# Optimization experiments

Hardware: AMD Instinct MI355X
Metric: run time of the kernel (lower is better)

## Reference

```python
import jax, jax.numpy as jnp
import numpy as np

N_NODES = 50000
N_EDGES = 800000
N_SUPPORTS = 2
D_IN = 512
D_OUT = 128


def setup_inputs() -> dict:
    key = jax.random.key(0)
    ks = jax.random.split(key, 6)
    x = jax.random.normal(ks[0], (N_NODES, D_IN), dtype=jnp.float32)
    kernels = jax.random.normal(ks[1], (N_SUPPORTS, D_IN, D_OUT), dtype=jnp.float32) * 0.05
    bias = jax.random.normal(ks[2], (D_OUT,), dtype=jnp.float32) * 0.05
    adj_vals = jax.random.uniform(ks[3], (N_SUPPORTS, N_EDGES), dtype=jnp.float32)
    adj_rows = jax.random.randint(ks[4], (N_SUPPORTS, N_EDGES), 0, N_NODES, dtype=jnp.int32)
    adj_cols = jax.random.randint(ks[5], (N_SUPPORTS, N_EDGES), 0, N_NODES, dtype=jnp.int32)
    return {"x": x, "kernels": kernels, "bias": bias,
            "adj_vals": adj_vals, "adj_rows": adj_rows, "adj_cols": adj_cols}


def _spmm(vals, rows, cols, dense):
    # COO sparse [N,N] @ dense [N,F] -> [N,F]
    gathered = vals[:, None] * dense[cols]            # [E, F]
    return jax.ops.segment_sum(gathered, rows, num_segments=N_NODES)


def reference(x, kernels, bias, adj_vals, adj_rows, adj_cols):
    # dropout rate = 0.0 -> identity
    out = jnp.zeros((N_NODES, D_OUT), dtype=x.dtype)
    for s in range(N_SUPPORTS):  # small fixed number of supports
        pre_sup = x @ kernels[s]                      # [N, D_OUT]
        out = out + _spmm(adj_vals[s], adj_rows[s], adj_cols[s], pre_sup)
    out = out + bias
    return jax.nn.relu(out)
```

## Files before the change

### kernel.cpp

```cpp
#include <hip/hip_runtime.h>

#define N_NODES 50000
#define N_EDGES 800000
#define D_IN    512
#define D_OUT   128
#define N_SUP   2
#define N_COLS  (N_SUP * D_OUT)
#define BINS    (N_SUP * N_NODES)
#define NB_S    196
#define NB      (N_SUP * NB_S)
#define CAP     4608
#define CHUNK   4096
#define NCHUNK  ((N_EDGES + CHUNK - 1) / CHUNK)

typedef __attribute__((ext_vector_type(8))) __bf16 bf16x8;
typedef __attribute__((ext_vector_type(4))) float  f32x4;

__global__ __launch_bounds__(256) void convert_w(const float* __restrict__ w,
                                                 __bf16* __restrict__ wt2) {
    const int g = blockIdx.x * 256 + threadIdx.x;
    if (g >= (D_IN / 8) * N_COLS) return;
    const int kq = g >> 8;
    const int n  = g & 255;
    const int s  = n >> 7;
    const int np = n & 127;
    bf16x8 v;
#pragma unroll
    for (int j = 0; j < 8; ++j) {
        const int k = kq * 8 + j;
        v[j] = (__bf16)w[((size_t)s * D_IN + k) * D_OUT + np];
    }
    *(bf16x8*)(wt2 + (size_t)g * 8) = v;
}

__global__ __launch_bounds__(256) void gemm_bf16(const float* __restrict__ x,
                                                 const __bf16* __restrict__ wt2,
                                                 __bf16* __restrict__ pre) {
    __shared__ __align__(16) __bf16 Bs[2048 * 8];

    const int t    = threadIdx.x;
    const int lane = t & 63;
    const int w    = t >> 6;
    const int l15  = lane & 15;
    const int quad = lane >> 4;

    const int rbase = blockIdx.x * 64 + w * 16;
    int arow = rbase + l15;
    if (arow >= N_NODES) arow = N_NODES - 1;
    const float* aptr = x + (size_t)arow * D_IN + quad * 8;

    f32x4 acc[16];
#pragma unroll
    for (int i = 0; i < 16; ++i) acc[i] = (f32x4)0.f;

    for (int kb = 0; kb < 8; ++kb) {
        const __bf16* gsrc = wt2 + ((size_t)kb * 2048 + w * 64 + lane) * 8;
#pragma unroll
        for (int i = 0; i < 8; ++i) {
            __builtin_amdgcn_global_load_lds(
                (const __attribute__((address_space(1))) unsigned int*)(gsrc + (size_t)i * 2048),
                (__attribute__((address_space(3))) unsigned int*)(&Bs[(i * 256 + w * 64) * 8]),
                16, 0, 0);
        }
        bf16x8 afrag[2];
#pragma unroll
        for (int kk = 0; kk < 2; ++kk) {
            const float* ap = aptr + kb * 64 + kk * 32;
            float4 f0 = *(const float4*)(ap);
            float4 f1 = *(const float4*)(ap + 4);
            bf16x8 a;
            a[0] = (__bf16)f0.x; a[1] = (__bf16)f0.y;
            a[2] = (__bf16)f0.z; a[3] = (__bf16)f0.w;
            a[4] = (__bf16)f1.x; a[5] = (__bf16)f1.y;
            a[6] = (__bf16)f1.z; a[7] = (__bf16)f1.w;
            afrag[kk] = a;
        }
        __syncthreads();

#pragma unroll
        for (int kk = 0; kk < 2; ++kk) {
            const __bf16* bbase = &Bs[((kk * 4 + quad) * 256 + l15) * 8];
#pragma unroll
            for (int ct = 0; ct < 16; ++ct) {
                bf16x8 b = *(const bf16x8*)(bbase + ct * 128);
                acc[ct] = __builtin_amdgcn_mfma_f32_16x16x32_bf16(afrag[kk], b, acc[ct], 0, 0, 0);
            }
        }
        __syncthreads();
    }

#pragma unroll
    for (int ct = 0; ct < 16; ++ct) {
        const int col = ct * 16 + l15;
        const int s   = col >> 7;
        const int cp  = col & 127;
#pragma unroll
        for (int r = 0; r < 4; ++r) {
            const int row = rbase + quad * 4 + r;
            if (row < N_NODES)
                pre[((size_t)s * N_NODES + row) * D_OUT + cp] = (__bf16)acc[ct][r];
        }
    }
}

__global__ __launch_bounds__(256) void scatter_coarse(const float* __restrict__ adj_vals,
                                                      const int* __restrict__ adj_rows,
                                                      const int* __restrict__ adj_cols,
                                                      int* __restrict__ gcursor,
                                                      uint2* __restrict__ coarse) {
    __shared__ int lh[NB_S];
    __shared__ int lbase[NB_S];
    const int s = blockIdx.y;
    const int t = threadIdx.x;
    if (t < NB_S) lh[t] = 0;
    __syncthreads();

    const int e0 = blockIdx.x * CHUNK;
    int   rr[16]; int cc[16]; float vv[16];
#pragma unroll
    for (int i = 0; i < 16; ++i) {
        const int e = e0 + i * 256 + t;
        if (e < N_EDGES) {
            const size_t src = (size_t)s * N_EDGES + e;
            rr[i] = adj_rows[src];
            cc[i] = adj_cols[src];
            vv[i] = adj_vals[src];
            atomicAdd(&lh[rr[i] >> 8], 1);
        } else {
            rr[i] = -1; cc[i] = 0; vv[i] = 0.f;
        }
    }
    __syncthreads();
    if (t < NB_S) {
        lbase[t] = lh[t] ? atomicAdd(&gcursor[s * NB_S + t], lh[t]) : 0;
        lh[t] = 0;
    }
    __syncthreads();
#pragma unroll
    for (int i = 0; i < 16; ++i) {
        if (rr[i] >= 0) {
            const int b    = rr[i] >> 8;
            const int pos  = lbase[b] + atomicAdd(&lh[b], 1);
            if (pos < CAP)
                coarse[(size_t)(s * NB_S + b) * CAP + pos] =
                    make_uint2(__float_as_uint(vv[i]),
                               ((unsigned)(rr[i] & 255) << 16) | (unsigned)cc[i]);
        }
    }
}

__global__ __launch_bounds__(256) void scatter_fine(const uint2* __restrict__ coarse,
                                                    const int* __restrict__ gcursor,
                                                    uint2* __restrict__ sorted,
                                                    int* __restrict__ row_off,
                                                    int* __restrict__ row_cnt) {
    __shared__ int rh[256];
    __shared__ int sd[256];
    __shared__ int rbs[256];
    __shared__ int rc[256];
    const int bk = blockIdx.x;
    const int s  = blockIdx.y;
    const int t  = threadIdx.x;
    const int bkt = s * NB_S + bk;
    const int b0  = bkt * CAP;
    const int cnt = min(gcursor[bkt], CAP);

    rh[t] = 0; rc[t] = 0;
    __syncthreads();
    for (int i = t; i < cnt; i += 256) {
        const uint2 ed = coarse[b0 + i];
        atomicAdd(&rh[ed.y >> 16], 1);
    }
    __syncthreads();
    const int myc = rh[t];
    sd[t] = myc;
    __syncthreads();
    for (int off = 1; off < 256; off <<= 1) {
        const int a = (t >= off) ? sd[t - off] : 0;
        __syncthreads();
        sd[t] += a;
        __syncthreads();
    }
    const int ex  = sd[t] - myc;
    const int row = (bk << 8) + t;
    if (row < N_NODES) {
        row_off[s * N_NODES + row] = b0 + ex;
        row_cnt[s * N_NODES + row] = myc;
    }
    rbs[t] = b0 + ex;
    __syncthreads();
    for (int i = t; i < cnt; i += 256) {
        const uint2 ed = coarse[b0 + i];
        const int   rl = ed.y >> 16;
        const int rank = atomicAdd(&rc[rl], 1);
        sorted[rbs[rl] + rank] = make_uint2(ed.x, ed.y & 0xFFFFu);
    }
}

__global__ __launch_bounds__(256) void gather_spmm(const int* __restrict__ row_off,
                                                   const int* __restrict__ row_cnt,
                                                   const uint2* __restrict__ sorted,
                                                   const uint4* __restrict__ pre_q,
                                                   const float* __restrict__ bias,
                                                   float* __restrict__ out) {
    const int lane = threadIdx.x & 63;
    const int q    = lane >> 4;
    const int fl   = lane & 15;
    const int row  = blockIdx.x * 4 + (threadIdx.x >> 6);
    if (row >= N_NODES) return;

    float a[8];
#pragma unroll
    for (int k = 0; k < 8; ++k) a[k] = 0.f;

#pragma unroll
    for (int s = 0; s < N_SUP; ++s) {
        const int bin   = s * N_NODES + row;
        const int start = row_off[bin];
        const int cnt   = row_cnt[bin];
        const uint4* psup = pre_q + (size_t)s * N_NODES * 16 + fl;

        for (int e0 = 0; e0 < cnt; e0 += 64) {
            const int m = min(64, cnt - e0);
            int   c = 0;
            float v = 0.f;
            if (lane < m) {
                const uint2 ed = sorted[start + e0 + lane];
                v = __uint_as_float(ed.x);
                c = (int)ed.y;
            }
            const int steps = (m + 3) >> 2;

            auto step = [&](int jj) {
                const int   idx = (jj < m) ? jj : 0;
                float vj = __shfl(v, idx);
                const int cj = __shfl(c, idx);
                if (jj >= m) vj = 0.f;
                const uint4 p = psup[(size_t)cj * 16];
                a[0] += vj * __uint_as_float(p.x << 16);
                a[1] += vj * __uint_as_float(p.x & 0xffff0000u);
                a[2] += vj * __uint_as_float(p.y << 16);
                a[3] += vj * __uint_as_float(p.y & 0xffff0000u);
                a[4] += vj * __uint_as_float(p.z << 16);
                a[5] += vj * __uint_as_float(p.z & 0xffff0000u);
                a[6] += vj * __uint_as_float(p.w << 16);
                a[7] += vj * __uint_as_float(p.w & 0xffff0000u);
            };
            int jj = 0;
            for (; jj + 1 < steps; jj += 2) {
                step(jj * 4 + q);
                step(jj * 4 + 4 + q);
            }
            if (jj < steps) step(jj * 4 + q);
        }
    }

#pragma unroll
    for (int k = 0; k < 8; ++k) {
        a[k] += __shfl_xor(a[k], 16);
        a[k] += __shfl_xor(a[k], 32);
    }

    if (lane < 16) {
        const float4 b0 = *(const float4*)(bias + fl * 8);
        const float4 b1 = *(const float4*)(bias + fl * 8 + 4);
        float4 o0, o1;
        o0.x = fmaxf(a[0] + b0.x, 0.f);
        o0.y = fmaxf(a[1] + b0.y, 0.f);
        o0.z = fmaxf(a[2] + b0.z, 0.f);
        o0.w = fmaxf(a[3] + b0.w, 0.f);
        o1.x = fmaxf(a[4] + b1.x, 0.f);
        o1.y = fmaxf(a[5] + b1.y, 0.f);
        o1.z = fmaxf(a[6] + b1.z, 0.f);
        o1.w = fmaxf(a[7] + b1.w, 0.f);
        float* dst = out + (size_t)row * D_OUT + fl * 8;
        *(float4*)(dst)     = o0;
        *(float4*)(dst + 4) = o1;
    }
}

extern "C" void kernel_launch(void* const* d_in, const int* in_sizes, int n_in,
                              void* d_out, int out_size, void* d_ws, size_t ws_size,
                              hipStream_t stream) {
    const float* x        = (const float*)d_in[0];
    const float* kernels  = (const float*)d_in[1];
    const float* bias     = (const float*)d_in[2];
    const float* adj_vals = (const float*)d_in[3];
    const int*   adj_rows = (const int*)d_in[4];
    const int*   adj_cols = (const int*)d_in[5];
    float* out = (float*)d_out;

    char* ws = (char*)d_ws;
    size_t off = 0;
    auto alloc = [&](size_t bytes) {
        char* p = ws + off;
        off += (bytes + 255) & ~(size_t)255;
        return p;
    };
    __bf16* pre    = (__bf16*)alloc(sizeof(__bf16) * N_SUP * N_NODES * D_OUT);
    __bf16* wt2    = (__bf16*)alloc(sizeof(__bf16) * D_IN * N_COLS);
    uint2*  coarse = (uint2*) alloc(sizeof(uint2)  * NB * CAP);
    uint2*  sorted = (uint2*) alloc(sizeof(uint2)  * NB * CAP);
    int*    row_off = (int*)alloc(sizeof(int) * BINS);
    int*    row_cnt = (int*)alloc(sizeof(int) * BINS);
    int*    gcursor = (int*)alloc(sizeof(int) * NB);

    convert_w<<<(D_IN / 8) * N_COLS / 256, 256, 0, stream>>>(kernels, wt2);
    gemm_bf16<<<(N_NODES + 63) / 64, 256, 0, stream>>>(x, wt2, pre);

    hipMemsetAsync(gcursor, 0, sizeof(int) * NB, stream);
    dim3 gc(NCHUNK, N_SUP);
    scatter_coarse<<<gc, 256, 0, stream>>>(adj_vals, adj_rows, adj_cols, gcursor, coarse);
    dim3 gf(NB_S, N_SUP);
    scatter_fine<<<gf, 256, 0, stream>>>(coarse, gcursor, sorted, row_off, row_cnt);

    gather_spmm<<<(N_NODES + 3) / 4, 256, 0, stream>>>(row_off, row_cnt, sorted,
                                                       (const uint4*)pre, bias, out);
}
```

Baseline: 283.8 us.

## Stage bucket scatters in LDS for coalesced writes; fold cursor reset into convert_w

Both scatter passes now sort their edges by bucket or row inside shared memory first, then write them out contiguously. This replaces random per-edge global stores with coalesced ones. scatter_fine now loads its edges into registers once instead of reading coarse twice, and the gcursor memset is folded into convert_w to save one launch. The cost is much larger LDS use per block (32 KB and 36 KB), which lowers occupancy, and extra block-wide scans and barriers.

```diff
diff --git a/kernel.cpp b/kernel.cpp
--- a/kernel.cpp
+++ b/kernel.cpp
@@ -17,8 +17,10 @@
 typedef __attribute__((ext_vector_type(4))) float  f32x4;
 
 __global__ __launch_bounds__(256) void convert_w(const float* __restrict__ w,
-                                                 __bf16* __restrict__ wt2) {
+                                                 __bf16* __restrict__ wt2,
+                                                 int* __restrict__ gcursor) {
     const int g = blockIdx.x * 256 + threadIdx.x;
+    if (g < NB) gcursor[g] = 0;
     if (g >= (D_IN / 8) * N_COLS) return;
     const int kq = g >> 8;
     const int n  = g & 255;
@@ -108,11 +110,16 @@
                                                       const int* __restrict__ adj_cols,
                                                       int* __restrict__ gcursor,
                                                       uint2* __restrict__ coarse) {
-    __shared__ int lh[NB_S];
+    __shared__ int hist[NB_S];
+    __shared__ int excl[NB_S];
     __shared__ int lbase[NB_S];
+    __shared__ int rankc[NB_S];
+    __shared__ int sc[256];
+    __shared__ uint2 buf[CHUNK];
+
     const int s = blockIdx.y;
     const int t = threadIdx.x;
-    if (t < NB_S) lh[t] = 0;
+    if (t < NB_S) { hist[t] = 0; rankc[t] = 0; }
     __syncthreads();
 
     const int e0 = blockIdx.x * CHUNK;
@@ -125,27 +132,45 @@
             rr[i] = adj_rows[src];
             cc[i] = adj_cols[src];
             vv[i] = adj_vals[src];
-            atomicAdd(&lh[rr[i] >> 8], 1);
+            atomicAdd(&hist[rr[i] >> 8], 1);
         } else {
             rr[i] = -1; cc[i] = 0; vv[i] = 0.f;
         }
     }
     __syncthreads();
+
+    sc[t] = (t < NB_S) ? hist[t] : 0;
+    __syncthreads();
+    for (int off = 1; off < 256; off <<= 1) {
+        const int a = (t >= off) ? sc[t - off] : 0;
+        __syncthreads();
+        sc[t] += a;
+        __syncthreads();
+    }
     if (t < NB_S) {
-        lbase[t] = lh[t] ? atomicAdd(&gcursor[s * NB_S + t], lh[t]) : 0;
-        lh[t] = 0;
-    }
-    __syncthreads();
+        excl[t]  = sc[t] - hist[t];
+        lbase[t] = hist[t] ? atomicAdd(&gcursor[s * NB_S + t], hist[t]) : 0;
+    }
+    __syncthreads();
+
 #pragma unroll
     for (int i = 0; i < 16; ++i) {
         if (rr[i] >= 0) {
-            const int b    = rr[i] >> 8;
-            const int pos  = lbase[b] + atomicAdd(&lh[b], 1);
-            if (pos < CAP)
-                coarse[(size_t)(s * NB_S + b) * CAP + pos] =
-                    make_uint2(__float_as_uint(vv[i]),
-                               ((unsigned)(rr[i] & 255) << 16) | (unsigned)cc[i]);
-        }
+            const int b   = rr[i] >> 8;
+            const int pos = excl[b] + atomicAdd(&rankc[b], 1);
+            buf[pos] = make_uint2(__float_as_uint(vv[i]),
+                                  ((unsigned)rr[i] << 16) | (unsigned)cc[i]);
+        }
+    }
+    __syncthreads();
+
+    const int total = min(e0 + CHUNK, N_EDGES) - e0;
+    for (int i = t; i < total; i += 256) {
+        const uint2 ed = buf[i];
+        const int b   = ed.y >> 24;
+        const int dst = lbase[b] + (i - excl[b]);
+        if (dst < CAP)
+            coarse[(size_t)(s * NB_S + b) * CAP + dst] = ed;
     }
 }
 
@@ -156,22 +181,31 @@
                                                     int* __restrict__ row_cnt) {
     __shared__ int rh[256];
     __shared__ int sd[256];
-    __shared__ int rbs[256];
+    __shared__ int rex[256];
     __shared__ int rc[256];
+    __shared__ uint2 buf[CAP];
+
     const int bk = blockIdx.x;
     const int s  = blockIdx.y;
     const int t  = threadIdx.x;
     const int bkt = s * NB_S + bk;
-    const int b0  = bkt * CAP;
+    const size_t b0 = (size_t)bkt * CAP;
     const int cnt = min(gcursor[bkt], CAP);
 
     rh[t] = 0; rc[t] = 0;
     __syncthreads();
-    for (int i = t; i < cnt; i += 256) {
-        const uint2 ed = coarse[b0 + i];
-        atomicAdd(&rh[ed.y >> 16], 1);
-    }
-    __syncthreads();
+
+    uint2 ev[18];
+#pragma unroll
+    for (int j = 0; j < 18; ++j) {
+        const int i = j * 256 + t;
+        if (i < cnt) {
+            ev[j] = coarse[b0 + i];
+            atomicAdd(&rh[(ev[j].y >> 16) & 255], 1);
+        }
+    }
+    __syncthreads();
+
     const int myc = rh[t];
     sd[t] = myc;
     __syncthreads();
@@ -181,20 +215,28 @@
         sd[t] += a;
         __syncthreads();
     }
-    const int ex  = sd[t] - myc;
+    const int ex = sd[t] - myc;
+    rex[t] = ex;
     const int row = (bk << 8) + t;
     if (row < N_NODES) {
-        row_off[s * N_NODES + row] = b0 + ex;
+        row_off[s * N_NODES + row] = (int)(b0 + ex);
         row_cnt[s * N_NODES + row] = myc;
     }
-    rbs[t] = b0 + ex;
-    __syncthreads();
-    for (int i = t; i < cnt; i += 256) {
-        const uint2 ed = coarse[b0 + i];
-        const int   rl = ed.y >> 16;
-        const int rank = atomicAdd(&rc[rl], 1);
-        sorted[rbs[rl] + rank] = make_uint2(ed.x, ed.y & 0xFFFFu);
-    }
+    __syncthreads();
+
+#pragma unroll
+    for (int j = 0; j < 18; ++j) {
+        const int i = j * 256 + t;
+        if (i < cnt) {
+            const int rl   = (ev[j].y >> 16) & 255;
+            const int pos  = rex[rl] + atomicAdd(&rc[rl], 1);
+            buf[pos] = make_uint2(ev[j].x, ev[j].y & 0xFFFFu);
+        }
+    }
+    __syncthreads();
+
+    for (int i = t; i < cnt; i += 256)
+        sorted[b0 + i] = buf[i];
 }
 
 __global__ __launch_bounds__(256) void gather_spmm(const int* __restrict__ row_off,
@@ -305,10 +347,9 @@
     int*    row_cnt = (int*)alloc(sizeof(int) * BINS);
     int*    gcursor = (int*)alloc(sizeof(int) * NB);
 
-    convert_w<<<(D_IN / 8) * N_COLS / 256, 256, 0, stream>>>(kernels, wt2);
+    convert_w<<<(D_IN / 8) * N_COLS / 256, 256, 0, stream>>>(kernels, wt2, gcursor);
     gemm_bf16<<<(N_NODES + 63) / 64, 256, 0, stream>>>(x, wt2, pre);
 
-    hipMemsetAsync(gcursor, 0, sizeof(int) * NB, stream);
     dim3 gc(NCHUNK, N_SUP);
     scatter_coarse<<<gc, 256, 0, stream>>>(adj_vals, adj_rows, adj_cols, gcursor, coarse);
     dim3 gf(NB_S, N_SUP);
```

New measurement: 276.5 us. -2.5%, faster.
